# Kernel tuning notes

Hardware: AMD Instinct MI355X
Metric: run time of the kernel (lower is better)

The kernel has to match this reference:

```python
import jax, jax.numpy as jnp
import numpy as np

DIM = 1024
HEADS = 16
HEAD_DIM = DIM // HEADS
B, N = 8, 1024


def setup_inputs() -> dict:
    key = jax.random.key(0)
    ks = jax.random.split(key, 10)
    s = lambda fan_in: 1.0 / np.sqrt(fan_in)
    return {
        "x": jax.random.normal(ks[0], (B, N, DIM), jnp.float32),
        "pose_angles": jax.random.normal(ks[1], (B, 3), jnp.float32),
        # weights stored (in, out) so y = x @ W + b (equivalent to torch Linear)
        "Wqkv": jax.random.normal(ks[2], (DIM, 3 * DIM), jnp.float32) * s(DIM),
        "bqkv": jnp.zeros((3 * DIM,), jnp.float32),
        "W1": jax.random.normal(ks[3], (3, 64), jnp.float32) * s(3),
        "b1": jnp.zeros((64,), jnp.float32),
        "W2": jax.random.normal(ks[4], (64, 3 * DIM), jnp.float32) * s(64),
        "b2": jnp.zeros((3 * DIM,), jnp.float32),
        "Wproj": jax.random.normal(ks[5], (DIM, DIM), jnp.float32) * s(DIM),
        "bproj": jnp.zeros((DIM,), jnp.float32),
    }


def reference(x, pose_angles, Wqkv, bqkv, W1, b1, W2, b2, Wproj, bproj):
    Bq, Nq, C = x.shape
    H, D = HEADS, HEAD_DIM
    # qkv projection -> [B,N,3,H,D] -> [3,B,H,N,D]
    qkv = (x @ Wqkv + bqkv).reshape(Bq, Nq, 3, H, D).transpose(2, 0, 3, 1, 4)
    q, k, v = qkv[0], qkv[1], qkv[2]
    # pose MLP: 3 -> 64 -> 3*dim, chunked into per-head biases [B,H,1,D]
    pose_emb = jax.nn.relu(pose_angles @ W1 + b1) @ W2 + b2
    pose_q, pose_k, pose_v = jnp.split(pose_emb, 3, axis=1)
    pose_q = pose_q.reshape(Bq, H, 1, D)
    pose_k = pose_k.reshape(Bq, H, 1, D)
    pose_v = pose_v.reshape(Bq, H, 1, D)
    q = q + pose_q
    k = k + pose_k
    v = v + pose_v
    scale = 1.0 / jnp.sqrt(jnp.asarray(D, x.dtype))
    attn = jax.nn.softmax(jnp.einsum("bhnd,bhmd->bhnm", q, k) * scale, axis=-1)
    # dropout is identity in eval mode
    out = jnp.einsum("bhnm,bhmd->bhnd", attn, v)
    out = out.transpose(0, 2, 1, 3).reshape(Bq, Nq, C)
    return out @ Wproj + bproj
```

## Files before the change

kernel.cpp:

```cpp
#include <hip/hip_runtime.h>
#include <stdint.h>

typedef unsigned short u16;
typedef short bf16x8 __attribute__((ext_vector_type(8)));
typedef short bf16x4 __attribute__((ext_vector_type(4)));
typedef float f32x4 __attribute__((ext_vector_type(4)));
typedef u16 u16x4 __attribute__((ext_vector_type(4)));

__device__ __forceinline__ u16 f2bf(float f) {
  union { float f; unsigned int u; } v; v.f = f;
  unsigned int r = v.u + 0x7fffu + ((v.u >> 16) & 1u);
  return (u16)(r >> 16);
}

__device__ __forceinline__ void async16(const void* g, void* l) {
  __builtin_amdgcn_global_load_lds(
      (const __attribute__((address_space(1))) unsigned int*)g,
      (__attribute__((address_space(3))) unsigned int*)l, 16, 0, 0);
}

__device__ __forceinline__ f32x4 mfma16x16(bf16x4 a, bf16x4 b, f32x4 c) {
#if __has_builtin(__builtin_amdgcn_mfma_f32_16x16x16bf16_1k)
  return __builtin_amdgcn_mfma_f32_16x16x16bf16_1k(a, b, c, 0, 0, 0);
#else
  asm volatile("v_mfma_f32_16x16x16_bf16 %0, %1, %2, %0\n\ts_nop 7\n\ts_nop 7"
               : "+v"(c) : "v"(a), "v"(b));
  return c;
#endif
}

__global__ void __launch_bounds__(256) front_kernel(
    const float4* __restrict__ x4, u16x4* __restrict__ xh4,
    const float* __restrict__ ang, const float* __restrict__ W1,
    const float* __restrict__ b1, const float* __restrict__ W2,
    const float* __restrict__ b2, float* __restrict__ pose,
    const float* __restrict__ Wqkv, u16* __restrict__ wqkvt,
    const float* __restrict__ Wproj, u16* __restrict__ wprojt) {
  __shared__ float sh[64 * 65];
  const int fb = blockIdx.x, t = threadIdx.x;
  if (fb < 96) {
    float (*hid)[64] = (float (*)[64])sh;
    for (int idx = t; idx < 512; idx += 256) {
      int b = idx >> 6, j = idx & 63;
      float a = b1[j];
#pragma unroll
      for (int i = 0; i < 3; ++i) a += ang[b * 3 + i] * W1[i * 64 + j];
      hid[b][j] = fmaxf(a, 0.f);
    }
    __syncthreads();
    int idx = fb * 256 + t;
    int b = idx / 3072, c = idx - b * 3072;
    float a = b2[c];
#pragma unroll
    for (int j = 0; j < 64; ++j) a += hid[b][j] * W2[j * 3072 + c];
    pose[idx] = a;
  } else if (fb < 1120) {
    const int n4 = 8 * 1024 * 1024 / 4;
    int i = (fb - 96) * 256 + t;
    const int stride = 1024 * 256;
    for (; i < n4; i += stride) {
      float4 v = x4[i];
      u16x4 o;
      o[0] = f2bf(v.x); o[1] = f2bf(v.y); o[2] = f2bf(v.z); o[3] = f2bf(v.w);
      xh4[i] = o;
    }
  } else {
    const float* W; u16* Wt; int Kdim, Ncol, bx, by;
    if (fb < 1888) { W = Wqkv; Wt = wqkvt; Kdim = 1024; Ncol = 3072;
                     int b = fb - 1120; bx = b % 48; by = b / 48; }
    else           { W = Wproj; Wt = wprojt; Kdim = 1024; Ncol = 1024;
                     int b = fb - 1888; bx = b % 16; by = b / 16; }
    float (*tile)[65] = (float (*)[65])sh;
    const int tx = t & 63, ty = t >> 6;
    const int c0 = bx * 64, k0 = by * 64;
#pragma unroll
    for (int rr = 0; rr < 16; ++rr) {
      int row = rr * 4 + ty;
      tile[row][tx] = W[(size_t)(k0 + row) * Ncol + c0 + tx];
    }
    __syncthreads();
#pragma unroll
    for (int rr = 0; rr < 16; ++rr) {
      int row = rr * 4 + ty;
      Wt[(size_t)(c0 + row) * Kdim + k0 + tx] = f2bf(tile[tx][row]);
    }
  }
}

template <int EPI>
__global__ void __launch_bounds__(512) gemm8_kernel(
    const u16* __restrict__ A, const u16* __restrict__ Bt,
    const float* __restrict__ bias, const float* __restrict__ pose,
    u16* __restrict__ qout, u16* __restrict__ kout, u16* __restrict__ vtout,
    float* __restrict__ cout, int Kdim, int Ncols, int nTilesX) {
  constexpr int BOFF = 256 * 64;
  __shared__ u16 lds[2][(256 + 128) * 64];
  const int t = threadIdx.x, l = t & 63, w = t >> 6;
  const int g = l >> 4, r16 = l & 15;
  const int wr = w >> 1, wc = w & 1;
  const int xk = r16 & 7;
  const int nwg = gridDim.x, cpx = nwg >> 3;
  const int swz = (blockIdx.x & 7) * cpx + (blockIdx.x >> 3);
  const int n0 = (swz % nTilesX) * 128, m0 = (swz / nTilesX) * 256;
  const u16* Ab = A + (size_t)m0 * Kdim;
  const u16* Bb = Bt + (size_t)n0 * Kdim;

  auto stage = [&](int buf, int kt, int st) {
#pragma unroll
    for (int it = 0; it < 2; ++it) {
      int idx = it * 512 + t, row = idx >> 3;
      int seg = (idx & 7) ^ (row & 7);
      if (st < 2)
        async16(Ab + (size_t)(st * 128 + row) * Kdim + kt + seg * 8,
                &lds[buf][st * 128 * 64 + idx * 8]);
      else
        async16(Bb + (size_t)row * Kdim + kt + seg * 8, &lds[buf][BOFF + idx * 8]);
    }
  };

  f32x4 acc[4][4] = {};
  const int nT = Kdim >> 6;
#pragma unroll
  for (int st = 0; st < 3; ++st) stage(0, 0, st);

  for (int tt = 0; tt < nT; ++tt) {
    const int cur = tt & 1, nxt = cur ^ 1;
    const bool pf = (tt + 1 < nT);
    const int ktn = (tt + 1) << 6;
    if (pf) {
      stage(nxt, ktn, 0);
      __builtin_amdgcn_sched_barrier(0);
      asm volatile("s_waitcnt vmcnt(2)" ::: "memory");
    } else {
      asm volatile("s_waitcnt vmcnt(0)" ::: "memory");
    }
    __builtin_amdgcn_s_barrier();
    __builtin_amdgcn_sched_barrier(0);
    bf16x8 bfr[4][2], af[2][2];
#pragma unroll
    for (int nj = 0; nj < 4; ++nj)
#pragma unroll
      for (int ks = 0; ks < 2; ++ks)
        bfr[nj][ks] = *(const bf16x8*)&lds[cur][BOFF + (wc * 64 + nj * 16 + r16) * 64 +
                                               ((ks * 4 + g) ^ xk) * 8];
#pragma unroll
    for (int mi = 0; mi < 2; ++mi)
#pragma unroll
      for (int ks = 0; ks < 2; ++ks)
        af[mi][ks] = *(const bf16x8*)&lds[cur][(wr * 64 + mi * 16 + r16) * 64 +
                                              ((ks * 4 + g) ^ xk) * 8];
    __builtin_amdgcn_s_setprio(1);
#pragma unroll
    for (int ks = 0; ks < 2; ++ks)
#pragma unroll
      for (int mi = 0; mi < 2; ++mi)
#pragma unroll
        for (int nj = 0; nj < 4; ++nj)
          acc[mi][nj] = __builtin_amdgcn_mfma_f32_16x16x32_bf16(af[mi][ks], bfr[nj][ks],
                                                                acc[mi][nj], 0, 0, 0);
    __builtin_amdgcn_s_setprio(0);
    if (pf) { stage(nxt, ktn, 1); stage(nxt, ktn, 2); }
    bf16x8 af2[2][2];
#pragma unroll
    for (int mi = 0; mi < 2; ++mi)
#pragma unroll
      for (int ks = 0; ks < 2; ++ks)
        af2[mi][ks] = *(const bf16x8*)&lds[cur][(wr * 64 + (mi + 2) * 16 + r16) * 64 +
                                               ((ks * 4 + g) ^ xk) * 8];
    __builtin_amdgcn_s_setprio(1);
#pragma unroll
    for (int ks = 0; ks < 2; ++ks)
#pragma unroll
      for (int mi = 0; mi < 2; ++mi)
#pragma unroll
        for (int nj = 0; nj < 4; ++nj)
          acc[mi + 2][nj] = __builtin_amdgcn_mfma_f32_16x16x32_bf16(af2[mi][ks], bfr[nj][ks],
                                                                    acc[mi + 2][nj], 0, 0, 0);
    __builtin_amdgcn_s_setprio(0);
    __builtin_amdgcn_s_barrier();
  }

#pragma unroll
  for (int mi = 0; mi < 4; ++mi)
#pragma unroll
    for (int nj = 0; nj < 4; ++nj)
#pragma unroll
      for (int r = 0; r < 4; ++r) {
        int row = m0 + wr * 64 + mi * 16 + g * 4 + r;
        int col = n0 + wc * 64 + nj * 16 + r16;
        float v = acc[mi][nj][r] + bias[col];
        if (EPI == 0) {
          int b = row >> 10, n = row & 1023;
          v += pose[b * 3072 + col];
          u16 hv = f2bf(v);
          int three = col >> 10, hh = (col >> 6) & 15, d = col & 63;
          size_t bhh = (size_t)(b * 16 + hh);
          if (three == 0)      qout[(bhh * 1024 + n) * 64 + d] = hv;
          else if (three == 1) kout[(bhh * 1024 + n) * 64 + d] = hv;
          else                 vtout[(bhh * 64 + d) * 1024 + n] = hv;
        } else {
          cout[(size_t)row * Ncols + col] = v;
        }
      }
}

__global__ void __launch_bounds__(256) attn_kernel(
    const u16* __restrict__ Qb, const u16* __restrict__ Kb,
    const u16* __restrict__ Vtb, u16* __restrict__ aout) {
  __shared__ u16 ldsK[64][72];
  __shared__ u16 ldsV[64][72];
  const int t = threadIdx.x, l = t & 63, w = t >> 6;
  const int g = l >> 4, r16 = l & 15;
  const int blk = blockIdx.x;
  const int bh = blk & 127, qt = blk >> 7;
  const int b = bh >> 4, h = bh & 15;
  const int q0 = qt * 64 + w * 16;
  const u16* Qp = Qb + ((size_t)bh * 1024 + q0 + r16) * 64;
  bf16x8 qreg0 = *(const bf16x8*)(Qp + g * 8);
  bf16x8 qreg1 = *(const bf16x8*)(Qp + 32 + g * 8);
  const u16* Kbase = Kb + (size_t)bh * 1024 * 64;
  const u16* Vbase = Vtb + (size_t)bh * 64 * 1024;
  float m = -1e30f, rs = 0.f;
  f32x4 o[4] = {};
  for (int key0 = 0; key0 < 1024; key0 += 64) {
#pragma unroll
    for (int ii = 0; ii < 2; ++ii) {
      int idx = ii * 256 + t, row = idx >> 3, seg = idx & 7;
      *(bf16x8*)&ldsK[row][seg * 8] = *(const bf16x8*)(Kbase + (size_t)(key0 + row) * 64 + seg * 8);
      *(bf16x8*)&ldsV[row][seg * 8] = *(const bf16x8*)(Vbase + (size_t)row * 1024 + key0 + seg * 8);
    }
    __syncthreads();
    f32x4 s[4] = {};
#pragma unroll
    for (int f = 0; f < 4; ++f) {
      bf16x8 ak0 = *(const bf16x8*)&ldsK[f * 16 + r16][g * 8];
      s[f] = __builtin_amdgcn_mfma_f32_16x16x32_bf16(ak0, qreg0, s[f], 0, 0, 0);
      bf16x8 ak1 = *(const bf16x8*)&ldsK[f * 16 + r16][32 + g * 8];
      s[f] = __builtin_amdgcn_mfma_f32_16x16x32_bf16(ak1, qreg1, s[f], 0, 0, 0);
    }
    float mt = -1e30f;
#pragma unroll
    for (int f = 0; f < 4; ++f)
#pragma unroll
      for (int r = 0; r < 4; ++r) { s[f][r] *= 0.125f; mt = fmaxf(mt, s[f][r]); }
    mt = fmaxf(mt, __shfl_xor(mt, 16));
    mt = fmaxf(mt, __shfl_xor(mt, 32));
    float mnew = fmaxf(m, mt);
    float alpha = __expf(m - mnew);
    float rt = 0.f;
    bf16x4 pa[4];
#pragma unroll
    for (int f = 0; f < 4; ++f) {
#pragma unroll
      for (int r = 0; r < 4; ++r) {
        float p = __expf(s[f][r] - mnew);
        rt += p;
        pa[f][r] = (short)f2bf(p);
      }
    }
    rt += __shfl_xor(rt, 16);
    rt += __shfl_xor(rt, 32);
    rs = rs * alpha + rt;
    m = mnew;
    float ar[4];
#pragma unroll
    for (int r = 0; r < 4; ++r) ar[r] = __shfl(alpha, (l & 48) | (g * 4 + r));
#pragma unroll
    for (int nf = 0; nf < 4; ++nf)
#pragma unroll
      for (int r = 0; r < 4; ++r) o[nf][r] *= ar[r];
#pragma unroll
    for (int s4 = 0; s4 < 4; ++s4)
#pragma unroll
      for (int nf = 0; nf < 4; ++nf) {
        bf16x4 bv = *(const bf16x4*)&ldsV[nf * 16 + r16][s4 * 16 + g * 4];
        o[nf] = mfma16x16(pa[s4], bv, o[nf]);
      }
    __syncthreads();
  }
  float rr[4];
#pragma unroll
  for (int r = 0; r < 4; ++r) rr[r] = __shfl(1.0f / rs, (l & 48) | (g * 4 + r));
#pragma unroll
  for (int nf = 0; nf < 4; ++nf)
#pragma unroll
    for (int r = 0; r < 4; ++r) {
      int qq = qt * 64 + w * 16 + g * 4 + r;
      int d = nf * 16 + r16;
      aout[((size_t)b * 1024 + qq) * 1024 + h * 64 + d] = f2bf(o[nf][r] * rr[r]);
    }
}

extern "C" void kernel_launch(void* const* d_in, const int* in_sizes, int n_in,
                              void* d_out, int out_size, void* d_ws, size_t ws_size,
                              hipStream_t stream) {
  (void)in_sizes; (void)n_in; (void)out_size; (void)ws_size;
  const float* x     = (const float*)d_in[0];
  const float* ang   = (const float*)d_in[1];
  const float* Wqkv  = (const float*)d_in[2];
  const float* bqkv  = (const float*)d_in[3];
  const float* W1    = (const float*)d_in[4];
  const float* b1    = (const float*)d_in[5];
  const float* W2    = (const float*)d_in[6];
  const float* b2    = (const float*)d_in[7];
  const float* Wproj = (const float*)d_in[8];
  const float* bproj = (const float*)d_in[9];
  float* out = (float*)d_out;
  char* ws = (char*)d_ws;

  u16* xh     = (u16*)(ws);
  u16* wqkvt  = (u16*)(ws + (size_t)16 * 1024 * 1024);
  u16* wprojt = (u16*)(ws + (size_t)22 * 1024 * 1024);
  float* pose = (float*)(ws + (size_t)24 * 1024 * 1024);
  u16* Qb     = (u16*)(ws + (size_t)25 * 1024 * 1024);
  u16* Kb     = (u16*)(ws + (size_t)41 * 1024 * 1024);
  u16* Vtb    = (u16*)(ws + (size_t)57 * 1024 * 1024);

  front_kernel<<<2144, 256, 0, stream>>>((const float4*)x, (u16x4*)xh,
                                         ang, W1, b1, W2, b2, pose,
                                         Wqkv, wqkvt, Wproj, wprojt);
  gemm8_kernel<0><<<768, 512, 0, stream>>>(xh, wqkvt, bqkv, pose,
                                           Qb, Kb, Vtb, nullptr, 1024, 3072, 24);
  attn_kernel<<<2048, 256, 0, stream>>>(Qb, Kb, Vtb, xh);
  gemm8_kernel<1><<<256, 512, 0, stream>>>(xh, wprojt, bproj, nullptr,
                                           nullptr, nullptr, nullptr, out, 1024, 1024, 8);
}
```

Baseline: 198.0 us.

## Double-buffer K/V tiles and use lazy rescaling with exp2 in attention

The attention loop now prefetches the next K/V tile into registers while computing on the current LDS buffer, then writes it into a second LDS buffer, so each tile needs one barrier instead of two. The softmax folds the 1/8 scale into an exp2 constant and skips the running-max rescale of the output accumulators unless the new tile max exceeds the old one by more than a threshold. This hides global load latency behind the MFMA work and cuts exp and multiply work, in exchange for doubled LDS use, more live registers, and a wave-wide vote.

```diff
diff --git a/kernel.cpp b/kernel.cpp
--- a/kernel.cpp
+++ b/kernel.cpp
@@ -207,8 +207,8 @@
 __global__ void __launch_bounds__(256) attn_kernel(
     const u16* __restrict__ Qb, const u16* __restrict__ Kb,
     const u16* __restrict__ Vtb, u16* __restrict__ aout) {
-  __shared__ u16 ldsK[64][72];
-  __shared__ u16 ldsV[64][72];
+  __shared__ u16 ldsK[2][64][72];
+  __shared__ u16 ldsV[2][64][72];
   const int t = threadIdx.x, l = t & 63, w = t >> 6;
   const int g = l >> 4, r16 = l & 15;
   const int blk = blockIdx.x;
@@ -220,63 +220,86 @@
   bf16x8 qreg1 = *(const bf16x8*)(Qp + 32 + g * 8);
   const u16* Kbase = Kb + (size_t)bh * 1024 * 64;
   const u16* Vbase = Vtb + (size_t)bh * 64 * 1024;
-  float m = -1e30f, rs = 0.f;
+  const float cexp = 0.18033688f;
+
+  const int row0 = t >> 3, seg0 = t & 7;
+  const int row1 = (256 + t) >> 3, seg1 = t & 7;
+  bf16x8 kreg0, kreg1, vreg0, vreg1;
+  auto gload = [&](int key0) {
+    kreg0 = *(const bf16x8*)(Kbase + (size_t)(key0 + row0) * 64 + seg0 * 8);
+    vreg0 = *(const bf16x8*)(Vbase + (size_t)row0 * 1024 + key0 + seg0 * 8);
+    kreg1 = *(const bf16x8*)(Kbase + (size_t)(key0 + row1) * 64 + seg1 * 8);
+    vreg1 = *(const bf16x8*)(Vbase + (size_t)row1 * 1024 + key0 + seg1 * 8);
+  };
+  auto lwrite = [&](int buf) {
+    *(bf16x8*)&ldsK[buf][row0][seg0 * 8] = kreg0;
+    *(bf16x8*)&ldsV[buf][row0][seg0 * 8] = vreg0;
+    *(bf16x8*)&ldsK[buf][row1][seg1 * 8] = kreg1;
+    *(bf16x8*)&ldsV[buf][row1][seg1 * 8] = vreg1;
+  };
+
+  float m = -3e38f, rs = 0.f;
   f32x4 o[4] = {};
-  for (int key0 = 0; key0 < 1024; key0 += 64) {
-#pragma unroll
-    for (int ii = 0; ii < 2; ++ii) {
-      int idx = ii * 256 + t, row = idx >> 3, seg = idx & 7;
-      *(bf16x8*)&ldsK[row][seg * 8] = *(const bf16x8*)(Kbase + (size_t)(key0 + row) * 64 + seg * 8);
-      *(bf16x8*)&ldsV[row][seg * 8] = *(const bf16x8*)(Vbase + (size_t)row * 1024 + key0 + seg * 8);
-    }
-    __syncthreads();
+  gload(0); lwrite(0);
+  __syncthreads();
+  int cur = 0;
+  for (int kt = 0; kt < 16; ++kt) {
+    const bool pf = (kt + 1 < 16);
+    if (pf) gload((kt + 1) * 64);
     f32x4 s[4] = {};
 #pragma unroll
     for (int f = 0; f < 4; ++f) {
-      bf16x8 ak0 = *(const bf16x8*)&ldsK[f * 16 + r16][g * 8];
+      bf16x8 ak0 = *(const bf16x8*)&ldsK[cur][f * 16 + r16][g * 8];
       s[f] = __builtin_amdgcn_mfma_f32_16x16x32_bf16(ak0, qreg0, s[f], 0, 0, 0);
-      bf16x8 ak1 = *(const bf16x8*)&ldsK[f * 16 + r16][32 + g * 8];
+      bf16x8 ak1 = *(const bf16x8*)&ldsK[cur][f * 16 + r16][32 + g * 8];
       s[f] = __builtin_amdgcn_mfma_f32_16x16x32_bf16(ak1, qreg1, s[f], 0, 0, 0);
     }
-    float mt = -1e30f;
-#pragma unroll
-    for (int f = 0; f < 4; ++f)
-#pragma unroll
-      for (int r = 0; r < 4; ++r) { s[f][r] *= 0.125f; mt = fmaxf(mt, s[f][r]); }
+    float m01, m23, mt = -3e38f;
+#pragma unroll
+    for (int f = 0; f < 4; ++f) {
+      m01 = fmaxf(s[f][0], s[f][1]);
+      m23 = fmaxf(s[f][2], s[f][3]);
+      mt = fmaxf(mt, fmaxf(m01, m23));
+    }
     mt = fmaxf(mt, __shfl_xor(mt, 16));
     mt = fmaxf(mt, __shfl_xor(mt, 32));
-    float mnew = fmaxf(m, mt);
-    float alpha = __expf(m - mnew);
+    if (!__all(mt - m <= 64.f)) {
+      float mnew = fmaxf(m, mt);
+      float alpha = exp2f((m - mnew) * cexp);
+      float ar[4];
+#pragma unroll
+      for (int r = 0; r < 4; ++r) ar[r] = __shfl(alpha, (l & 48) | (g * 4 + r));
+#pragma unroll
+      for (int nf = 0; nf < 4; ++nf)
+#pragma unroll
+        for (int r = 0; r < 4; ++r) o[nf][r] *= ar[r];
+      rs *= alpha;
+      m = mnew;
+    }
     float rt = 0.f;
     bf16x4 pa[4];
 #pragma unroll
     for (int f = 0; f < 4; ++f) {
 #pragma unroll
       for (int r = 0; r < 4; ++r) {
-        float p = __expf(s[f][r] - mnew);
+        float p = exp2f((s[f][r] - m) * cexp);
         rt += p;
         pa[f][r] = (short)f2bf(p);
       }
     }
     rt += __shfl_xor(rt, 16);
     rt += __shfl_xor(rt, 32);
-    rs = rs * alpha + rt;
-    m = mnew;
-    float ar[4];
-#pragma unroll
-    for (int r = 0; r < 4; ++r) ar[r] = __shfl(alpha, (l & 48) | (g * 4 + r));
-#pragma unroll
-    for (int nf = 0; nf < 4; ++nf)
-#pragma unroll
-      for (int r = 0; r < 4; ++r) o[nf][r] *= ar[r];
+    rs += rt;
 #pragma unroll
     for (int s4 = 0; s4 < 4; ++s4)
 #pragma unroll
       for (int nf = 0; nf < 4; ++nf) {
-        bf16x4 bv = *(const bf16x4*)&ldsV[nf * 16 + r16][s4 * 16 + g * 4];
+        bf16x4 bv = *(const bf16x4*)&ldsV[cur][nf * 16 + r16][s4 * 16 + g * 4];
         o[nf] = mfma16x16(pa[s4], bv, o[nf]);
       }
+    if (pf) lwrite(cur ^ 1);
     __syncthreads();
+    cur ^= 1;
   }
   float rr[4];
 #pragma unroll
```

Result: no change. 200.8 us (+1.4%).
